# Performance work log

Hardware: AMD Instinct MI355X
Metric: run time of the kernel (lower is better)

The kernel has to match this reference:

```python
import jax, jax.numpy as jnp
import numpy as np
from jax import lax

DIM = 192
HEADS = 8
HID = int(DIM * 4.0)

def setup_inputs() -> dict:
    key = jax.random.key(0)
    ks = jax.random.split(key, 10)
    b, c, h, w = 4, DIM, 256, DIM  # w must equal dim for the Mlp over last axis
    x = jax.random.normal(ks[0], (b, c, h, w), dtype=jnp.float32)
    return {
        "x": x,
        "ln1_w": jnp.ones((DIM,), jnp.float32),
        "ln1_b": jnp.zeros((DIM,), jnp.float32),
        "temperature": jnp.ones((HEADS, 1, 1), jnp.float32),
        "qkv_w": jax.random.normal(ks[1], (3 * DIM, DIM), jnp.float32) * 0.02,
        "dw_w": jax.random.normal(ks[2], (3 * DIM, 1, 3, 3), jnp.float32) * 0.1,
        "proj_w": jax.random.normal(ks[3], (DIM, DIM), jnp.float32) * 0.02,
        "ln2_w": jnp.ones((DIM,), jnp.float32),
        "ln2_b": jnp.zeros((DIM,), jnp.float32),
        "fc1_w": jax.random.normal(ks[4], (HID, DIM), jnp.float32) * 0.02,
        "fc1_b": jnp.zeros((HID,), jnp.float32),
        "fc2_w": jax.random.normal(ks[5], (DIM, HID), jnp.float32) * 0.02,
        "fc2_b": jnp.zeros((DIM,), jnp.float32),
    }

def _layernorm_chan(x, w, b):
    # WithBias LayerNorm over the channel axis, per spatial location (to_3d -> LN -> to_4d)
    mu = jnp.mean(x, axis=1, keepdims=True)
    var = jnp.mean((x - mu) ** 2, axis=1, keepdims=True)
    y = (x - mu) / jnp.sqrt(var + 1e-5)
    return y * w[None, :, None, None] + b[None, :, None, None]

def _l2norm(x, axis=-1, eps=1e-12):
    n = jnp.sqrt(jnp.sum(x * x, axis=axis, keepdims=True))
    return x / jnp.maximum(n, eps)

def _attention(x, temperature, qkv_w, dw_w, proj_w):
    b, c, h, w = x.shape
    # 1x1 conv (pointwise GEMM) then 3x3 depthwise conv
    qkv = jnp.einsum('oc,bchw->bohw', qkv_w, x)
    qkv = lax.conv_general_dilated(qkv, dw_w, window_strides=(1, 1), padding='SAME',
                                   feature_group_count=3 * c,
                                   dimension_numbers=('NCHW', 'OIHW', 'NCHW'))
    q, k, v = jnp.split(qkv, 3, axis=1)
    ch = c // HEADS
    q = q.reshape(b, HEADS, ch, h * w)
    k = k.reshape(b, HEADS, ch, h * w)
    v = v.reshape(b, HEADS, ch, h * w)
    q = _l2norm(q)
    k = _l2norm(k)
    attn = jnp.einsum('bhcn,bhdn->bhcd', q, k) * temperature  # [b,H,ch,ch] channel attention
    attn = jax.nn.softmax(attn, axis=-1)
    out = jnp.einsum('bhcd,bhdn->bhcn', attn, v).reshape(b, c, h, w)
    return jnp.einsum('oc,bchw->bohw', proj_w, out)

def _mlp(x, fc1_w, fc1_b, fc2_w, fc2_b):
    # nn.Linear applied on the LAST axis (w == dim), matching the original quirk
    h1 = jnp.einsum('bchw,ow->bcho', x, fc1_w) + fc1_b
    h1 = jax.nn.gelu(h1, approximate=False)
    return jnp.einsum('bcho,do->bchd', h1, fc2_w) + fc2_b

def reference(x, ln1_w, ln1_b, temperature, qkv_w, dw_w, proj_w, ln2_w, ln2_b, fc1_w, fc1_b, fc2_w, fc2_b):
    x = x + _attention(_layernorm_chan(x, ln1_w, ln1_b), temperature, qkv_w, dw_w, proj_w)
    x = x + _mlp(_layernorm_chan(x, ln2_w, ln2_b), fc1_w, fc1_b, fc2_w, fc2_b)
    return x
```

## Files before the change

kernel.cpp:

```cpp
#include <hip/hip_runtime.h>
#include <math.h>

#define SSP   49152
#define HDIM  256
#define WDIM  192
#define CDIM  192
#define NHEAD 8
#define CH    24
#define OC3   576
#define HIDF  768
#define NB    4
#define SCCH  24

typedef short bf16x8 __attribute__((ext_vector_type(8)));
typedef short bf16x4 __attribute__((ext_vector_type(4)));
typedef float f32x4  __attribute__((ext_vector_type(4)));

__device__ inline short f2bf(float f) {
  unsigned u = __float_as_uint(f);
  u += 0x7fffu + ((u >> 16) & 1u);
  return (short)(u >> 16);
}
__device__ inline float bf2f(short h) {
  return __uint_as_float(((unsigned)(unsigned short)h) << 16);
}

__global__ __launch_bounds__(256) void cvt_bf16(const float* __restrict__ in,
                                                short* __restrict__ out, int n) {
  int i = blockIdx.x * 256 + threadIdx.x;
  if (i < n) out[i] = f2bf(in[i]);
}

__global__ __launch_bounds__(256) void ln_to_bf16T(const float* __restrict__ x,
                                                   const float* __restrict__ w,
                                                   const float* __restrict__ b,
                                                   short* __restrict__ yt) {
  int s = blockIdx.x * 256 + threadIdx.x;
  int bz = blockIdx.y;
  const float* xb = x + (size_t)bz * CDIM * SSP;
  float sum = 0.f, sq = 0.f;
  for (int c = 0; c < CDIM; ++c) {
    float v = xb[(size_t)c * SSP + s];
    sum += v; sq += v * v;
  }
  float mu = sum * (1.f / CDIM);
  float rstd = rsqrtf(sq * (1.f / CDIM) - mu * mu + 1e-5f);
  short* yp = yt + (size_t)bz * SSP * CDIM + (size_t)s * CDIM;
  for (int c8 = 0; c8 < CDIM / 8; ++c8) {
    bf16x8 v;
#pragma unroll
    for (int j = 0; j < 8; ++j) {
      int c = c8 * 8 + j;
      v[j] = f2bf((xb[(size_t)c * SSP + s] - mu) * rstd * w[c] + b[c]);
    }
    *(bf16x8*)(yp + c8 * 8) = v;
  }
}

__global__ __launch_bounds__(256) void ln_to_bf16N(const float* __restrict__ x,
                                                   const float* __restrict__ w,
                                                   const float* __restrict__ b,
                                                   short* __restrict__ y) {
  int s = blockIdx.x * 256 + threadIdx.x;
  int bz = blockIdx.y;
  const float* xb = x + (size_t)bz * CDIM * SSP;
  short* yb = y + (size_t)bz * CDIM * SSP;
  float sum = 0.f, sq = 0.f;
  for (int c = 0; c < CDIM; ++c) {
    float v = xb[(size_t)c * SSP + s];
    sum += v; sq += v * v;
  }
  float mu = sum * (1.f / CDIM);
  float rstd = rsqrtf(sq * (1.f / CDIM) - mu * mu + 1e-5f);
  for (int c = 0; c < CDIM; ++c) {
    float v = xb[(size_t)c * SSP + s];
    yb[(size_t)c * SSP + s] = f2bf((v - mu) * rstd * w[c] + b[c]);
  }
}

template <int BM, int BN, int WM, int WN, bool RESID, bool OUT_BF16>
__global__ __launch_bounds__(256) void mfma_gemm(
    const short* __restrict__ A, const short* __restrict__ B,
    const float* __restrict__ resid, void* __restrict__ Cv,
    int M, int N, int K, long long strideB, long long strideC) {
  constexpr int BK = 32, PAD = 40;
  constexpr int WTM = BM / WM, WTN = BN / WN;
  constexpr int FM = WTM / 16, FN = WTN / 16;
  static_assert(WM * WN == 4 && BM % 64 == 0 && BN % 64 == 0, "cfg");
  __shared__ short As[BM * PAD];
  __shared__ short Bs[BN * PAD];
  const int tid = threadIdx.x;
  const int m0 = blockIdx.y * BM, n0 = blockIdx.x * BN;
  const long long z = blockIdx.z;
  const short* Bz = B + z * strideB;
  const int w = tid >> 6, lane = tid & 63;
  const int wm = w / WN, wn = w % WN;
  const int r16 = lane & 15, kg = lane >> 4;
  const int arow = tid >> 2, akc = tid & 3;

  f32x4 acc[FM][FN] = {};

  for (int k0 = 0; k0 < K; k0 += BK) {
#pragma unroll
    for (int i = 0; i < BM; i += 64) {
      bf16x8 v = *(const bf16x8*)(A + (size_t)(m0 + i + arow) * K + k0 + akc * 8);
      *(bf16x8*)(&As[(i + arow) * PAD + akc * 8]) = v;
    }
#pragma unroll
    for (int i = 0; i < BN; i += 64) {
      bf16x8 v = *(const bf16x8*)(Bz + (size_t)(n0 + i + arow) * K + k0 + akc * 8);
      *(bf16x8*)(&Bs[(i + arow) * PAD + akc * 8]) = v;
    }
    __syncthreads();
    bf16x8 af[FM], bfr[FN];
#pragma unroll
    for (int i = 0; i < FM; ++i)
      af[i] = *(bf16x8*)(&As[(wm * WTM + i * 16 + r16) * PAD + kg * 8]);
#pragma unroll
    for (int j = 0; j < FN; ++j)
      bfr[j] = *(bf16x8*)(&Bs[(wn * WTN + j * 16 + r16) * PAD + kg * 8]);
#pragma unroll
    for (int i = 0; i < FM; ++i)
#pragma unroll
      for (int j = 0; j < FN; ++j)
        acc[i][j] = __builtin_amdgcn_mfma_f32_16x16x32_bf16(af[i], bfr[j], acc[i][j], 0, 0, 0);
    __syncthreads();
  }

  float* Cf = (float*)Cv + z * strideC;
  short* Ch = (short*)Cv + z * strideC;
  const float* R = RESID ? resid + z * strideC : nullptr;
#pragma unroll
  for (int i = 0; i < FM; ++i) {
#pragma unroll
    for (int j = 0; j < FN; ++j) {
#pragma unroll
      for (int t = 0; t < 4; ++t) {
        int m = m0 + wm * WTM + i * 16 + kg * 4 + t;
        int n = n0 + wn * WTN + j * 16 + r16;
        float v = acc[i][j][t];
        size_t idx = (size_t)m * N + n;
        if (RESID) v += R[idx];
        if (OUT_BF16) Ch[idx] = f2bf(v); else Cf[idx] = v;
      }
    }
  }
}

__global__ __launch_bounds__(256) void dwconv_tile(const short* __restrict__ in,
                                                   const float* __restrict__ w9,
                                                   short* __restrict__ out) {
  __shared__ short tile[34][208];
  const int tid = threadIdx.x;
  const int ch = blockIdx.x >> 3;
  const int slab = blockIdx.x & 7;
  const int o = ch % OC3;
  const int y0 = slab * 32;
  float wr[9];
#pragma unroll
  for (int i = 0; i < 9; ++i) wr[i] = w9[o * 9 + i];
  const short* ip = in + (size_t)ch * SSP;

  if (tid < 34) { tile[tid][7] = 0; tile[tid][200] = 0; }
#pragma unroll
  for (int i = 0; i < 4; ++i) {
    int idx = i * 256 + tid;
    if (idx < 816) {
      int row = idx / 24, cx = idx - row * 24;
      int gy = y0 + row - 1;
      bf16x8 v = {};
      if (gy >= 0 && gy < HDIM) v = *(const bf16x8*)(ip + gy * WDIM + cx * 8);
      *(bf16x8*)(&tile[row][8 + cx * 8]) = v;
    }
  }
  __syncthreads();

  short* op = out + (size_t)ch * SSP;
#pragma unroll
  for (int g = 0; g < 3; ++g) {
    int G = g * 256 + tid;
    int r = G / 24, cx = G - (G / 24) * 24;
    int cb = cx * 8 + 7;
    float a[10], b[10], c[10];
#pragma unroll
    for (int d = 0; d < 10; ++d) {
      a[d] = bf2f(tile[r][cb + d]);
      b[d] = bf2f(tile[r + 1][cb + d]);
      c[d] = bf2f(tile[r + 2][cb + d]);
    }
    bf16x8 ov;
#pragma unroll
    for (int j = 0; j < 8; ++j) {
      float acc = wr[0] * a[j] + wr[1] * a[j + 1] + wr[2] * a[j + 2]
                + wr[3] * b[j] + wr[4] * b[j + 1] + wr[5] * b[j + 2]
                + wr[6] * c[j] + wr[7] * c[j + 1] + wr[8] * c[j + 2];
      ov[j] = f2bf(acc);
    }
    *(bf16x8*)(op + (y0 + r) * WDIM + cx * 8) = ov;
  }
}

__global__ __launch_bounds__(256) void scores_stage1(const short* __restrict__ D,
                                                     float* __restrict__ pdot,
                                                     float* __restrict__ qss,
                                                     float* __restrict__ kss) {
  int ch = blockIdx.x, h = blockIdx.y, b = blockIdx.z;
  __shared__ float qs[24][260];
  __shared__ float ks[24][260];
  int tid = threadIdx.x;
  int w = tid >> 6, lane = tid & 63;
  int c0 = w * 6;
  float acc[6] = {0.f, 0.f, 0.f, 0.f, 0.f, 0.f};
  float ssacc = 0.f;
  const short* qb = D + ((size_t)b * OC3 + h * CH) * SSP;
  const short* kb = D + ((size_t)b * OC3 + CDIM + h * CH) * SSP;
  for (int it = 0; it < 8; ++it) {
    int s0 = ch * 2048 + it * 256;
#pragma unroll
    for (int p = 0; p < 3; ++p) {
      int u = p * 256 + tid;
      int row = u >> 5, col8 = u & 31;
      bf16x8 qv = *(const bf16x8*)(qb + (size_t)row * SSP + s0 + col8 * 8);
      bf16x8 kv = *(const bf16x8*)(kb + (size_t)row * SSP + s0 + col8 * 8);
#pragma unroll
      for (int j = 0; j < 8; ++j) {
        qs[row][col8 * 8 + j] = bf2f(qv[j]);
        ks[row][col8 * 8 + j] = bf2f(kv[j]);
      }
    }
    __syncthreads();
    if (w < 2 && lane < 24) {
      const float (*src)[260] = (w == 0) ? qs : ks;
      for (int s = 0; s < 256; s += 4) {
        float4 v = *(const float4*)&src[lane][s];
        ssacc += v.x * v.x + v.y * v.y + v.z * v.z + v.w * v.w;
      }
    }
    if (lane < 24) {
      for (int s = 0; s < 256; s += 4) {
        float4 kv = *(float4*)&ks[lane][s];
#pragma unroll
        for (int i = 0; i < 6; ++i) {
          float4 qv = *(float4*)&qs[c0 + i][s];
          acc[i] += qv.x * kv.x + qv.y * kv.y + qv.z * kv.z + qv.w * kv.w;
        }
      }
    }
    __syncthreads();
  }
  if (lane < 24) {
    float* pb = pdot + (size_t)b * (NHEAD * CH * CH * SCCH);
#pragma unroll
    for (int i = 0; i < 6; ++i)
      pb[(((size_t)h * CH + (c0 + i)) * CH + lane) * SCCH + ch] = acc[i];
    if (w == 0) qss[(((size_t)b * NHEAD + h) * CH + lane) * SCCH + ch] = ssacc;
    if (w == 1) kss[(((size_t)b * NHEAD + h) * CH + lane) * SCCH + ch] = ssacc;
  }
}

__global__ void scores_reduce(const float* __restrict__ pdot,
                              const float* __restrict__ qss,
                              const float* __restrict__ kss,
                              const float* __restrict__ temp,
                              float* __restrict__ atn) {
  int c = blockIdx.x, h = blockIdx.y, b = blockIdx.z;
  int tid = threadIdx.x;
  __shared__ float row[24];
  if (tid < 24) {
    const float* p = pdot + (size_t)b * (NHEAD * CH * CH * SCCH) +
                     (((size_t)h * CH + c) * CH + tid) * SCCH;
    float s = 0.f;
#pragma unroll
    for (int i = 0; i < SCCH; ++i) s += p[i];
    const float* pq = qss + (((size_t)b * NHEAD + h) * CH + c) * SCCH;
    const float* pk = kss + (((size_t)b * NHEAD + h) * CH + tid) * SCCH;
    float sq = 0.f, sk = 0.f;
#pragma unroll
    for (int i = 0; i < SCCH; ++i) { sq += pq[i]; sk += pk[i]; }
    float rq = 1.f / fmaxf(sqrtf(sq), 1e-12f);
    float rk = 1.f / fmaxf(sqrtf(sk), 1e-12f);
    row[tid] = s * rq * rk * temp[h];
  }
  __syncthreads();
  if (tid < 24) {
    float mx = -1e30f;
    for (int d = 0; d < 24; ++d) mx = fmaxf(mx, row[d]);
    float sum = 0.f;
    for (int d = 0; d < 24; ++d) sum += expf(row[d] - mx);
    atn[((size_t)b * NHEAD + h) * 576 + c * CH + tid] = expf(row[tid] - mx) / sum;
  }
}

__global__ __launch_bounds__(256) void attn_pv_bf16(const short* __restrict__ D,
                                                    const float* __restrict__ atn,
                                                    short* __restrict__ pvt) {
  int nb = blockIdx.x, h = blockIdx.y, b = blockIdx.z;
  __shared__ float aL[24][24];
  int tid = threadIdx.x;
  const float* ab = atn + ((size_t)b * NHEAD + h) * 576;
  for (int i = tid; i < 576; i += 256) aL[i / 24][i % 24] = ab[i];
  __syncthreads();
  int n = nb * 256 + tid;
  const short* vb = D + ((size_t)b * OC3 + 2 * CDIM + h * CH) * SSP + n;
  float vv[24];
#pragma unroll
  for (int d = 0; d < 24; ++d) vv[d] = bf2f(vb[(size_t)d * SSP]);
  short* ob = pvt + (size_t)b * SSP * CDIM + (size_t)n * CDIM + h * CH;
  bf16x8 o0, o1, o2;
#pragma unroll
  for (int cc = 0; cc < 24; ++cc) {
    float s = 0.f;
#pragma unroll
    for (int d = 0; d < 24; ++d) s += aL[cc][d] * vv[d];
    short bv = f2bf(s);
    if (cc < 8) o0[cc & 7] = bv; else if (cc < 16) o1[cc & 7] = bv; else o2[cc & 7] = bv;
  }
  *(bf16x8*)(ob) = o0;
  *(bf16x8*)(ob + 8) = o1;
  *(bf16x8*)(ob + 16) = o2;
}

__global__ __launch_bounds__(512) void mlp_fused(const short* __restrict__ y2,
                                                 const short* __restrict__ w1,
                                                 const short* __restrict__ w2,
                                                 const float* __restrict__ b1,
                                                 const float* __restrict__ b2,
                                                 float* __restrict__ out) {
  __shared__ short y2s[128 * 200];
  __shared__ short w1s[64 * 200];
  __shared__ short w2s[192 * 72];
  __shared__ short h1s[128 * 72];
  const int tid = threadIdx.x;
  const int m0 = blockIdx.x * 128;
  const int w = tid >> 6, lane = tid & 63;
  const int r16 = lane & 15, kg = lane >> 4;
  const int wm = w >> 1;
  const int wn = w & 1;

  const int u0 = tid, u1 = 512 + tid, u2 = 1024 + tid;
  const int s1r[3] = {u0 / 24, u1 / 24, u2 / 24};
  const int s1c[3] = {u0 % 24, u1 % 24, u2 % 24};
  const int s2r[3] = {u0 / 8, u1 / 8, u2 / 8};
  const int s2c[3] = {u0 % 8, u1 % 8, u2 % 8};

#pragma unroll
  for (int it = 0; it < 6; ++it) {
    int u = it * 512 + tid;
    int row = u / 24, cx = u % 24;
    bf16x8 v = *(const bf16x8*)(y2 + (size_t)(m0 + row) * CDIM + cx * 8);
    *(bf16x8*)(&y2s[row * 200 + cx * 8]) = v;
  }
#pragma unroll
  for (int it = 0; it < 3; ++it) {
    bf16x8 v = *(const bf16x8*)(w1 + (size_t)s1r[it] * CDIM + s1c[it] * 8);
    *(bf16x8*)(&w1s[s1r[it] * 200 + s1c[it] * 8]) = v;
    bf16x8 v2 = *(const bf16x8*)(w2 + (size_t)s2r[it] * HIDF + s2c[it] * 8);
    *(bf16x8*)(&w2s[s2r[it] * 72 + s2c[it] * 8]) = v2;
  }
  __syncthreads();

  f32x4 bacc[2][6] = {};
  bf16x8 rw1[3], rw2[3];

  for (int hc = 0; hc < 12; ++hc) {
    if (hc < 11) {
#pragma unroll
      for (int it = 0; it < 3; ++it) {
        rw1[it] = *(const bf16x8*)(w1 + (size_t)((hc + 1) * 64 + s1r[it]) * CDIM + s1c[it] * 8);
        rw2[it] = *(const bf16x8*)(w2 + (size_t)s2r[it] * HIDF + (hc + 1) * 64 + s2c[it] * 8);
      }
    }

    f32x4 pacc[2][2] = {};
#pragma unroll
    for (int ks = 0; ks < 6; ++ks) {
      bf16x8 af[2], bg[2];
#pragma unroll
      for (int i = 0; i < 2; ++i)
        af[i] = *(bf16x8*)(&y2s[(wm * 32 + i * 16 + r16) * 200 + ks * 32 + kg * 8]);
#pragma unroll
      for (int j = 0; j < 2; ++j)
        bg[j] = *(bf16x8*)(&w1s[(wn * 32 + j * 16 + r16) * 200 + ks * 32 + kg * 8]);
#pragma unroll
      for (int i = 0; i < 2; ++i)
#pragma unroll
        for (int j = 0; j < 2; ++j)
          pacc[i][j] = __builtin_amdgcn_mfma_f32_16x16x32_bf16(bg[j], af[i], pacc[i][j], 0, 0, 0);
    }
#pragma unroll
    for (int i = 0; i < 2; ++i) {
      int mr = wm * 32 + i * 16 + r16;
#pragma unroll
      for (int j = 0; j < 2; ++j) {
        int hid0 = wn * 32 + j * 16 + kg * 4;
        bf16x4 pk;
#pragma unroll
        for (int t = 0; t < 4; ++t) {
          float v = pacc[i][j][t] + b1[hc * 64 + hid0 + t];
          v = 0.5f * v * (1.f + erff(v * 0.70710678118654752f));
          pk[t] = f2bf(v);
        }
        *(bf16x4*)(&h1s[mr * 72 + hid0]) = pk;
      }
    }
    __syncthreads();

#pragma unroll
    for (int ks = 0; ks < 2; ++ks) {
      bf16x8 a2[2];
#pragma unroll
      for (int i = 0; i < 2; ++i)
        a2[i] = *(bf16x8*)(&h1s[(wm * 32 + i * 16 + r16) * 72 + ks * 32 + kg * 8]);
#pragma unroll
      for (int j = 0; j < 6; ++j) {
        bf16x8 b2g = *(bf16x8*)(&w2s[(wn * 96 + j * 16 + r16) * 72 + ks * 32 + kg * 8]);
#pragma unroll
        for (int i = 0; i < 2; ++i)
          bacc[i][j] = __builtin_amdgcn_mfma_f32_16x16x32_bf16(a2[i], b2g, bacc[i][j], 0, 0, 0);
      }
    }
    __syncthreads();

    if (hc < 11) {
#pragma unroll
      for (int it = 0; it < 3; ++it) {
        *(bf16x8*)(&w1s[s1r[it] * 200 + s1c[it] * 8]) = rw1[it];
        *(bf16x8*)(&w2s[s2r[it] * 72 + s2c[it] * 8]) = rw2[it];
      }
      __syncthreads();
    }
  }

#pragma unroll
  for (int i = 0; i < 2; ++i)
#pragma unroll
    for (int j = 0; j < 6; ++j)
#pragma unroll
      for (int t = 0; t < 4; ++t) {
        int m = m0 + wm * 32 + i * 16 + kg * 4 + t;
        int n = wn * 96 + j * 16 + r16;
        size_t idx = (size_t)m * CDIM + n;
        out[idx] = bacc[i][j][t] + b2[n] + out[idx];
      }
}

extern "C" void kernel_launch(void* const* d_in, const int* in_sizes, int n_in,
                              void* d_out, int out_size, void* d_ws, size_t ws_size,
                              hipStream_t stream) {
  const float* x      = (const float*)d_in[0];
  const float* ln1_w  = (const float*)d_in[1];
  const float* ln1_b  = (const float*)d_in[2];
  const float* temp   = (const float*)d_in[3];
  const float* qkv_w  = (const float*)d_in[4];
  const float* dw_w   = (const float*)d_in[5];
  const float* proj_w = (const float*)d_in[6];
  const float* ln2_w  = (const float*)d_in[7];
  const float* ln2_b  = (const float*)d_in[8];
  const float* fc1_w  = (const float*)d_in[9];
  const float* fc1_b  = (const float*)d_in[10];
  const float* fc2_w  = (const float*)d_in[11];
  const float* fc2_b  = (const float*)d_in[12];
  float* out = (float*)d_out;

  char* base = (char*)d_ws;
  short* wq  = (short*)base;
  short* wp  = wq + 110592;
  short* w1  = wp + 36864;
  short* w2  = w1 + 147456;
  float* pdot= (float*)(base + 890880);
  float* qss = (float*)(base + 2660352);
  float* kss = (float*)(base + 2734080);
  float* atn = (float*)(base + 2807808);
  short* Dv  = (short*)(base + 4194304);
  short* y1t = Dv;
  short* T   = (short*)(base + 230686720);
  short* pvt = T;
  short* y2  = (short*)(base + 457179136);

  cvt_bf16<<<dim3(432), 256, 0, stream>>>(qkv_w, wq, 110592);
  cvt_bf16<<<dim3(144), 256, 0, stream>>>(proj_w, wp, 36864);
  cvt_bf16<<<dim3(576), 256, 0, stream>>>(fc1_w, w1, 147456);
  cvt_bf16<<<dim3(576), 256, 0, stream>>>(fc2_w, w2, 147456);

  ln_to_bf16T<<<dim3(SSP / 256, NB), 256, 0, stream>>>(x, ln1_w, ln1_b, y1t);
  mfma_gemm<64, 256, 1, 4, false, true><<<dim3(SSP / 256, OC3 / 64, NB), 256, 0, stream>>>(
      wq, y1t, nullptr, T, OC3, SSP, CDIM, (long long)SSP * CDIM, (long long)OC3 * SSP);
  dwconv_tile<<<dim3(NB * OC3 * 8), 256, 0, stream>>>(T, dw_w, Dv);
  scores_stage1<<<dim3(SCCH, NHEAD, NB), 256, 0, stream>>>(Dv, pdot, qss, kss);
  scores_reduce<<<dim3(CH, NHEAD, NB), 64, 0, stream>>>(pdot, qss, kss, temp, atn);
  attn_pv_bf16<<<dim3(SSP / 256, NHEAD, NB), 256, 0, stream>>>(Dv, atn, pvt);
  mfma_gemm<64, 256, 1, 4, true, false><<<dim3(SSP / 256, CDIM / 64, NB), 256, 0, stream>>>(
      wp, pvt, x, out, CDIM, SSP, CDIM, (long long)SSP * CDIM, (long long)CDIM * SSP);
  ln_to_bf16N<<<dim3(SSP / 256, NB), 256, 0, stream>>>(out, ln2_w, ln2_b, y2);
  mlp_fused<<<dim3(196608 / 128), 512, 0, stream>>>(y2, w1, w2, fc1_b, fc2_b, out);
}
```

Baseline: 1.015 ms.

## Tile layernorm through shared memory, per-batch launches, double-buffer MLP weights, tanh GELU

Layernorm kernels now stage a 192x64 tile in shared memory with coalesced float4 loads instead of striding per thread. The attention pipeline is launched once per batch element, dropping the batch grid dimension, presumably so each batch's working set stays cache-resident. The fused MLP keeps its A fragments in registers, double-buffers the weight chunks in shared memory to remove one barrier per iteration, and replaces erf GELU with a tanh/exp approximation. The approximation changes numerics slightly, and per-batch launches add launch overhead.

```diff
diff --git a/kernel.cpp b/kernel.cpp
--- a/kernel.cpp
+++ b/kernel.cpp
@@ -31,50 +31,68 @@
   if (i < n) out[i] = f2bf(in[i]);
 }
 
-__global__ __launch_bounds__(256) void ln_to_bf16T(const float* __restrict__ x,
-                                                   const float* __restrict__ w,
-                                                   const float* __restrict__ b,
-                                                   short* __restrict__ yt) {
-  int s = blockIdx.x * 256 + threadIdx.x;
-  int bz = blockIdx.y;
-  const float* xb = x + (size_t)bz * CDIM * SSP;
-  float sum = 0.f, sq = 0.f;
-  for (int c = 0; c < CDIM; ++c) {
-    float v = xb[(size_t)c * SSP + s];
-    sum += v; sq += v * v;
-  }
-  float mu = sum * (1.f / CDIM);
-  float rstd = rsqrtf(sq * (1.f / CDIM) - mu * mu + 1e-5f);
-  short* yp = yt + (size_t)bz * SSP * CDIM + (size_t)s * CDIM;
-  for (int c8 = 0; c8 < CDIM / 8; ++c8) {
-    bf16x8 v;
-#pragma unroll
-    for (int j = 0; j < 8; ++j) {
-      int c = c8 * 8 + j;
-      v[j] = f2bf((xb[(size_t)c * SSP + s] - mu) * rstd * w[c] + b[c]);
-    }
-    *(bf16x8*)(yp + c8 * 8) = v;
-  }
-}
-
-__global__ __launch_bounds__(256) void ln_to_bf16N(const float* __restrict__ x,
-                                                   const float* __restrict__ w,
-                                                   const float* __restrict__ b,
-                                                   short* __restrict__ y) {
-  int s = blockIdx.x * 256 + threadIdx.x;
-  int bz = blockIdx.y;
-  const float* xb = x + (size_t)bz * CDIM * SSP;
-  short* yb = y + (size_t)bz * CDIM * SSP;
-  float sum = 0.f, sq = 0.f;
-  for (int c = 0; c < CDIM; ++c) {
-    float v = xb[(size_t)c * SSP + s];
-    sum += v; sq += v * v;
-  }
-  float mu = sum * (1.f / CDIM);
-  float rstd = rsqrtf(sq * (1.f / CDIM) - mu * mu + 1e-5f);
-  for (int c = 0; c < CDIM; ++c) {
-    float v = xb[(size_t)c * SSP + s];
-    yb[(size_t)c * SSP + s] = f2bf((v - mu) * rstd * w[c] + b[c]);
+template <bool TRANS>
+__global__ __launch_bounds__(256) void ln_bf16(const float* __restrict__ xb,
+                                               const float* __restrict__ w,
+                                               const float* __restrict__ bia,
+                                               short* __restrict__ outb) {
+  __shared__ float xs[192][68];
+  __shared__ float ps[4][64], pq[4][64], mus[64], rst[64];
+  const int tid = threadIdx.x;
+  const int s0 = blockIdx.x * 64;
+#pragma unroll
+  for (int it = 0; it < 12; ++it) {
+    int u = it * 256 + tid;
+    int c = u >> 4, q = u & 15;
+    float4 v = *(const float4*)(xb + (size_t)c * SSP + s0 + q * 4);
+    *(float4*)&xs[c][q * 4] = v;
+  }
+  __syncthreads();
+  {
+    int s = tid & 63, p = tid >> 6;
+    float sm = 0.f, sq = 0.f;
+    for (int c = p * 48; c < p * 48 + 48; ++c) {
+      float v = xs[c][s]; sm += v; sq += v * v;
+    }
+    ps[p][s] = sm; pq[p][s] = sq;
+  }
+  __syncthreads();
+  if (tid < 64) {
+    float sm = ps[0][tid] + ps[1][tid] + ps[2][tid] + ps[3][tid];
+    float sq = pq[0][tid] + pq[1][tid] + pq[2][tid] + pq[3][tid];
+    float mu = sm * (1.f / CDIM);
+    mus[tid] = mu;
+    rst[tid] = rsqrtf(sq * (1.f / CDIM) - mu * mu + 1e-5f);
+  }
+  __syncthreads();
+  if (TRANS) {
+#pragma unroll
+    for (int it = 0; it < 6; ++it) {
+      int u = it * 256 + tid;
+      int c8 = u >> 6, sr = u & 63;
+      float mu = mus[sr], r = rst[sr];
+      bf16x8 o;
+#pragma unroll
+      for (int j = 0; j < 8; ++j) {
+        int c = c8 * 8 + j;
+        o[j] = f2bf((xs[c][sr] - mu) * r * w[c] + bia[c]);
+      }
+      *(bf16x8*)(outb + (size_t)(s0 + sr) * CDIM + c8 * 8) = o;
+    }
+  } else {
+#pragma unroll
+    for (int it = 0; it < 6; ++it) {
+      int u = it * 256 + tid;
+      int c = u >> 3, sv = u & 7;
+      float wc = w[c], bc = bia[c];
+      bf16x8 o;
+#pragma unroll
+      for (int j = 0; j < 8; ++j) {
+        int s = sv * 8 + j;
+        o[j] = f2bf((xs[c][s] - mus[s]) * rst[s] * wc + bc);
+      }
+      *(bf16x8*)(outb + (size_t)c * SSP + s0 + sv * 8) = o;
+    }
   }
 }
 
@@ -82,7 +100,7 @@
 __global__ __launch_bounds__(256) void mfma_gemm(
     const short* __restrict__ A, const short* __restrict__ B,
     const float* __restrict__ resid, void* __restrict__ Cv,
-    int M, int N, int K, long long strideB, long long strideC) {
+    int M, int N, int K) {
   constexpr int BK = 32, PAD = 40;
   constexpr int WTM = BM / WM, WTN = BN / WN;
   constexpr int FM = WTM / 16, FN = WTN / 16;
@@ -91,8 +109,6 @@
   __shared__ short Bs[BN * PAD];
   const int tid = threadIdx.x;
   const int m0 = blockIdx.y * BM, n0 = blockIdx.x * BN;
-  const long long z = blockIdx.z;
-  const short* Bz = B + z * strideB;
   const int w = tid >> 6, lane = tid & 63;
   const int wm = w / WN, wn = w % WN;
   const int r16 = lane & 15, kg = lane >> 4;
@@ -108,7 +124,7 @@
     }
 #pragma unroll
     for (int i = 0; i < BN; i += 64) {
-      bf16x8 v = *(const bf16x8*)(Bz + (size_t)(n0 + i + arow) * K + k0 + akc * 8);
+      bf16x8 v = *(const bf16x8*)(B + (size_t)(n0 + i + arow) * K + k0 + akc * 8);
       *(bf16x8*)(&Bs[(i + arow) * PAD + akc * 8]) = v;
     }
     __syncthreads();
@@ -127,9 +143,8 @@
     __syncthreads();
   }
 
-  float* Cf = (float*)Cv + z * strideC;
-  short* Ch = (short*)Cv + z * strideC;
-  const float* R = RESID ? resid + z * strideC : nullptr;
+  float* Cf = (float*)Cv;
+  short* Ch = (short*)Cv;
 #pragma unroll
   for (int i = 0; i < FM; ++i) {
 #pragma unroll
@@ -140,7 +155,7 @@
         int n = n0 + wn * WTN + j * 16 + r16;
         float v = acc[i][j][t];
         size_t idx = (size_t)m * N + n;
-        if (RESID) v += R[idx];
+        if (RESID) v += resid[idx];
         if (OUT_BF16) Ch[idx] = f2bf(v); else Cf[idx] = v;
       }
     }
@@ -154,11 +169,10 @@
   const int tid = threadIdx.x;
   const int ch = blockIdx.x >> 3;
   const int slab = blockIdx.x & 7;
-  const int o = ch % OC3;
   const int y0 = slab * 32;
   float wr[9];
 #pragma unroll
-  for (int i = 0; i < 9; ++i) wr[i] = w9[o * 9 + i];
+  for (int i = 0; i < 9; ++i) wr[i] = w9[ch * 9 + i];
   const short* ip = in + (size_t)ch * SSP;
 
   if (tid < 34) { tile[tid][7] = 0; tile[tid][200] = 0; }
@@ -204,7 +218,7 @@
                                                      float* __restrict__ pdot,
                                                      float* __restrict__ qss,
                                                      float* __restrict__ kss) {
-  int ch = blockIdx.x, h = blockIdx.y, b = blockIdx.z;
+  int ch = blockIdx.x, h = blockIdx.y;
   __shared__ float qs[24][260];
   __shared__ float ks[24][260];
   int tid = threadIdx.x;
@@ -212,8 +226,8 @@
   int c0 = w * 6;
   float acc[6] = {0.f, 0.f, 0.f, 0.f, 0.f, 0.f};
   float ssacc = 0.f;
-  const short* qb = D + ((size_t)b * OC3 + h * CH) * SSP;
-  const short* kb = D + ((size_t)b * OC3 + CDIM + h * CH) * SSP;
+  const short* qb = D + (size_t)(h * CH) * SSP;
+  const short* kb = D + (size_t)(CDIM + h * CH) * SSP;
   for (int it = 0; it < 8; ++it) {
     int s0 = ch * 2048 + it * 256;
 #pragma unroll
@@ -249,12 +263,11 @@
     __syncthreads();
   }
   if (lane < 24) {
-    float* pb = pdot + (size_t)b * (NHEAD * CH * CH * SCCH);
 #pragma unroll
     for (int i = 0; i < 6; ++i)
-      pb[(((size_t)h * CH + (c0 + i)) * CH + lane) * SCCH + ch] = acc[i];
-    if (w == 0) qss[(((size_t)b * NHEAD + h) * CH + lane) * SCCH + ch] = ssacc;
-    if (w == 1) kss[(((size_t)b * NHEAD + h) * CH + lane) * SCCH + ch] = ssacc;
+      pdot[(((size_t)h * CH + (c0 + i)) * CH + lane) * SCCH + ch] = acc[i];
+    if (w == 0) qss[((size_t)h * CH + lane) * SCCH + ch] = ssacc;
+    if (w == 1) kss[((size_t)h * CH + lane) * SCCH + ch] = ssacc;
   }
 }
 
@@ -263,17 +276,16 @@
                               const float* __restrict__ kss,
                               const float* __restrict__ temp,
                               float* __restrict__ atn) {
-  int c = blockIdx.x, h = blockIdx.y, b = blockIdx.z;
+  int c = blockIdx.x, h = blockIdx.y;
   int tid = threadIdx.x;
   __shared__ float row[24];
   if (tid < 24) {
-    const float* p = pdot + (size_t)b * (NHEAD * CH * CH * SCCH) +
-                     (((size_t)h * CH + c) * CH + tid) * SCCH;
+    const float* p = pdot + (((size_t)h * CH + c) * CH + tid) * SCCH;
     float s = 0.f;
 #pragma unroll
     for (int i = 0; i < SCCH; ++i) s += p[i];
-    const float* pq = qss + (((size_t)b * NHEAD + h) * CH + c) * SCCH;
-    const float* pk = kss + (((size_t)b * NHEAD + h) * CH + tid) * SCCH;
+    const float* pq = qss + ((size_t)h * CH + c) * SCCH;
+    const float* pk = kss + ((size_t)h * CH + tid) * SCCH;
     float sq = 0.f, sk = 0.f;
 #pragma unroll
     for (int i = 0; i < SCCH; ++i) { sq += pq[i]; sk += pk[i]; }
@@ -287,25 +299,25 @@
     for (int d = 0; d < 24; ++d) mx = fmaxf(mx, row[d]);
     float sum = 0.f;
     for (int d = 0; d < 24; ++d) sum += expf(row[d] - mx);
-    atn[((size_t)b * NHEAD + h) * 576 + c * CH + tid] = expf(row[tid] - mx) / sum;
+    atn[(size_t)h * 576 + c * CH + tid] = expf(row[tid] - mx) / sum;
   }
 }
 
 __global__ __launch_bounds__(256) void attn_pv_bf16(const short* __restrict__ D,
                                                     const float* __restrict__ atn,
                                                     short* __restrict__ pvt) {
-  int nb = blockIdx.x, h = blockIdx.y, b = blockIdx.z;
+  int nb = blockIdx.x, h = blockIdx.y;
   __shared__ float aL[24][24];
   int tid = threadIdx.x;
-  const float* ab = atn + ((size_t)b * NHEAD + h) * 576;
+  const float* ab = atn + (size_t)h * 576;
   for (int i = tid; i < 576; i += 256) aL[i / 24][i % 24] = ab[i];
   __syncthreads();
   int n = nb * 256 + tid;
-  const short* vb = D + ((size_t)b * OC3 + 2 * CDIM + h * CH) * SSP + n;
+  const short* vb = D + (size_t)(2 * CDIM + h * CH) * SSP + n;
   float vv[24];
 #pragma unroll
   for (int d = 0; d < 24; ++d) vv[d] = bf2f(vb[(size_t)d * SSP]);
-  short* ob = pvt + (size_t)b * SSP * CDIM + (size_t)n * CDIM + h * CH;
+  short* ob = pvt + (size_t)n * CDIM + h * CH;
   bf16x8 o0, o1, o2;
 #pragma unroll
   for (int cc = 0; cc < 24; ++cc) {
@@ -326,16 +338,13 @@
                                                  const float* __restrict__ b1,
                                                  const float* __restrict__ b2,
                                                  float* __restrict__ out) {
-  __shared__ short y2s[128 * 200];
-  __shared__ short w1s[64 * 200];
-  __shared__ short w2s[192 * 72];
-  __shared__ short h1s[128 * 72];
+  __shared__ short smem[62464];
+  short* h1s = smem + 53248;
   const int tid = threadIdx.x;
   const int m0 = blockIdx.x * 128;
   const int w = tid >> 6, lane = tid & 63;
   const int r16 = lane & 15, kg = lane >> 4;
-  const int wm = w >> 1;
-  const int wn = w & 1;
+  const int wm = w >> 1, wn = w & 1;
 
   const int u0 = tid, u1 = 512 + tid, u2 = 1024 + tid;
   const int s1r[3] = {u0 / 24, u1 / 24, u2 / 24};
@@ -343,26 +352,38 @@
   const int s2r[3] = {u0 / 8, u1 / 8, u2 / 8};
   const int s2c[3] = {u0 % 8, u1 % 8, u2 % 8};
 
+  short* y2s = smem + 26624;
 #pragma unroll
   for (int it = 0; it < 6; ++it) {
     int u = it * 512 + tid;
     int row = u / 24, cx = u % 24;
-    bf16x8 v = *(const bf16x8*)(y2 + (size_t)(m0 + row) * CDIM + cx * 8);
-    *(bf16x8*)(&y2s[row * 200 + cx * 8]) = v;
+    *(bf16x8*)(&y2s[row * 200 + cx * 8]) =
+        *(const bf16x8*)(y2 + (size_t)(m0 + row) * CDIM + cx * 8);
   }
 #pragma unroll
   for (int it = 0; it < 3; ++it) {
-    bf16x8 v = *(const bf16x8*)(w1 + (size_t)s1r[it] * CDIM + s1c[it] * 8);
-    *(bf16x8*)(&w1s[s1r[it] * 200 + s1c[it] * 8]) = v;
-    bf16x8 v2 = *(const bf16x8*)(w2 + (size_t)s2r[it] * HIDF + s2c[it] * 8);
-    *(bf16x8*)(&w2s[s2r[it] * 72 + s2c[it] * 8]) = v2;
-  }
-  __syncthreads();
+    *(bf16x8*)(&smem[s1r[it] * 200 + s1c[it] * 8]) =
+        *(const bf16x8*)(w1 + (size_t)s1r[it] * CDIM + s1c[it] * 8);
+    *(bf16x8*)(&smem[12800 + s2r[it] * 72 + s2c[it] * 8]) =
+        *(const bf16x8*)(w2 + (size_t)s2r[it] * HIDF + s2c[it] * 8);
+  }
+  __syncthreads();
+
+  bf16x8 afr[2][6];
+#pragma unroll
+  for (int ks = 0; ks < 6; ++ks)
+#pragma unroll
+    for (int i = 0; i < 2; ++i)
+      afr[i][ks] = *(bf16x8*)(&y2s[(wm * 32 + i * 16 + r16) * 200 + ks * 32 + kg * 8]);
 
   f32x4 bacc[2][6] = {};
   bf16x8 rw1[3], rw2[3];
 
   for (int hc = 0; hc < 12; ++hc) {
+    short* bw1 = smem + (hc & 1) * 26624;
+    short* bw2 = bw1 + 12800;
+    short* nw1 = smem + ((hc & 1) ^ 1) * 26624;
+    short* nw2 = nw1 + 12800;
     if (hc < 11) {
 #pragma unroll
       for (int it = 0; it < 3; ++it) {
@@ -370,22 +391,18 @@
         rw2[it] = *(const bf16x8*)(w2 + (size_t)s2r[it] * HIDF + (hc + 1) * 64 + s2c[it] * 8);
       }
     }
-
     f32x4 pacc[2][2] = {};
 #pragma unroll
     for (int ks = 0; ks < 6; ++ks) {
-      bf16x8 af[2], bg[2];
+      bf16x8 bg[2];
+#pragma unroll
+      for (int j = 0; j < 2; ++j)
+        bg[j] = *(bf16x8*)(&bw1[(wn * 32 + j * 16 + r16) * 200 + ks * 32 + kg * 8]);
 #pragma unroll
       for (int i = 0; i < 2; ++i)
-        af[i] = *(bf16x8*)(&y2s[(wm * 32 + i * 16 + r16) * 200 + ks * 32 + kg * 8]);
-#pragma unroll
-      for (int j = 0; j < 2; ++j)
-        bg[j] = *(bf16x8*)(&w1s[(wn * 32 + j * 16 + r16) * 200 + ks * 32 + kg * 8]);
-#pragma unroll
-      for (int i = 0; i < 2; ++i)
 #pragma unroll
         for (int j = 0; j < 2; ++j)
-          pacc[i][j] = __builtin_amdgcn_mfma_f32_16x16x32_bf16(bg[j], af[i], pacc[i][j], 0, 0, 0);
+          pacc[i][j] = __builtin_amdgcn_mfma_f32_16x16x32_bf16(bg[j], afr[i][ks], pacc[i][j], 0, 0, 0);
     }
 #pragma unroll
     for (int i = 0; i < 2; ++i) {
@@ -397,14 +414,14 @@
 #pragma unroll
         for (int t = 0; t < 4; ++t) {
           float v = pacc[i][j][t] + b1[hc * 64 + hid0 + t];
-          v = 0.5f * v * (1.f + erff(v * 0.70710678118654752f));
+          float u = v * (0.7978845608f + 0.0356774081f * v * v);
+          v = v / (1.f + __expf(-2.f * u));
           pk[t] = f2bf(v);
         }
         *(bf16x4*)(&h1s[mr * 72 + hid0]) = pk;
       }
     }
     __syncthreads();
-
 #pragma unroll
     for (int ks = 0; ks < 2; ++ks) {
       bf16x8 a2[2];
@@ -413,22 +430,20 @@
         a2[i] = *(bf16x8*)(&h1s[(wm * 32 + i * 16 + r16) * 72 + ks * 32 + kg * 8]);
 #pragma unroll
       for (int j = 0; j < 6; ++j) {
-        bf16x8 b2g = *(bf16x8*)(&w2s[(wn * 96 + j * 16 + r16) * 72 + ks * 32 + kg * 8]);
+        bf16x8 b2g = *(bf16x8*)(&bw2[(wn * 96 + j * 16 + r16) * 72 + ks * 32 + kg * 8]);
 #pragma unroll
         for (int i = 0; i < 2; ++i)
           bacc[i][j] = __builtin_amdgcn_mfma_f32_16x16x32_bf16(a2[i], b2g, bacc[i][j], 0, 0, 0);
       }
     }
+    if (hc < 11) {
+#pragma unroll
+      for (int it = 0; it < 3; ++it) {
+        *(bf16x8*)(&nw1[s1r[it] * 200 + s1c[it] * 8]) = rw1[it];
+        *(bf16x8*)(&nw2[s2r[it] * 72 + s2c[it] * 8]) = rw2[it];
+      }
+    }
     __syncthreads();
-
-    if (hc < 11) {
-#pragma unroll
-      for (int it = 0; it < 3; ++it) {
-        *(bf16x8*)(&w1s[s1r[it] * 200 + s1c[it] * 8]) = rw1[it];
-        *(bf16x8*)(&w2s[s2r[it] * 72 + s2c[it] * 8]) = rw2[it];
-      }
-      __syncthreads();
-    }
   }
 
 #pragma unroll
@@ -462,6 +477,8 @@
   const float* fc2_b  = (const float*)d_in[12];
   float* out = (float*)d_out;
 
+  const size_t BSZ  = (size_t)CDIM * SSP;
+  const size_t B3SZ = (size_t)OC3 * SSP;
   char* base = (char*)d_ws;
   short* wq  = (short*)base;
   short* wp  = wq + 110592;
@@ -482,15 +499,29 @@
   cvt_bf16<<<dim3(576), 256, 0, stream>>>(fc1_w, w1, 147456);
   cvt_bf16<<<dim3(576), 256, 0, stream>>>(fc2_w, w2, 147456);
 
-  ln_to_bf16T<<<dim3(SSP / 256, NB), 256, 0, stream>>>(x, ln1_w, ln1_b, y1t);
-  mfma_gemm<64, 256, 1, 4, false, true><<<dim3(SSP / 256, OC3 / 64, NB), 256, 0, stream>>>(
-      wq, y1t, nullptr, T, OC3, SSP, CDIM, (long long)SSP * CDIM, (long long)OC3 * SSP);
-  dwconv_tile<<<dim3(NB * OC3 * 8), 256, 0, stream>>>(T, dw_w, Dv);
-  scores_stage1<<<dim3(SCCH, NHEAD, NB), 256, 0, stream>>>(Dv, pdot, qss, kss);
-  scores_reduce<<<dim3(CH, NHEAD, NB), 64, 0, stream>>>(pdot, qss, kss, temp, atn);
-  attn_pv_bf16<<<dim3(SSP / 256, NHEAD, NB), 256, 0, stream>>>(Dv, atn, pvt);
-  mfma_gemm<64, 256, 1, 4, true, false><<<dim3(SSP / 256, CDIM / 64, NB), 256, 0, stream>>>(
-      wp, pvt, x, out, CDIM, SSP, CDIM, (long long)SSP * CDIM, (long long)CDIM * SSP);
-  ln_to_bf16N<<<dim3(SSP / 256, NB), 256, 0, stream>>>(out, ln2_w, ln2_b, y2);
+  for (int b = 0; b < NB; ++b) {
+    const float* xb  = x + (size_t)b * BSZ;
+    float* outb      = out + (size_t)b * BSZ;
+    short* y1tb      = y1t + (size_t)b * BSZ;
+    short* Tb        = T + (size_t)b * B3SZ;
+    short* Dvb       = Dv + (size_t)b * B3SZ;
+    short* pvtb      = pvt + (size_t)b * BSZ;
+    short* y2b       = y2 + (size_t)b * BSZ;
+    float* pdotb     = pdot + (size_t)b * (NHEAD * CH * CH * SCCH);
+    float* qssb      = qss + (size_t)b * (NHEAD * CH * SCCH);
+    float* kssb      = kss + (size_t)b * (NHEAD * CH * SCCH);
+    float* atnb      = atn + (size_t)b * (NHEAD * 576);
+
+    ln_bf16<true><<<dim3(SSP / 64), 256, 0, stream>>>(xb, ln1_w, ln1_b, y1tb);
+    mfma_gemm<64, 256, 1, 4, false, true><<<dim3(SSP / 256, OC3 / 64), 256, 0, stream>>>(
+        wq, y1tb, nullptr, Tb, OC3, SSP, CDIM);
+    dwconv_tile<<<dim3(OC3 * 8), 256, 0, stream>>>(Tb, dw_w, Dvb);
+    scores_stage1<<<dim3(SCCH, NHEAD), 256, 0, stream>>>(Dvb, pdotb, qssb, kssb);
+    scores_reduce<<<dim3(CH, NHEAD), 64, 0, stream>>>(pdotb, qssb, kssb, temp, atnb);
+    attn_pv_bf16<<<dim3(SSP / 256, NHEAD), 256, 0, stream>>>(Dvb, atnb, pvtb);
+    mfma_gemm<64, 256, 1, 4, true, false><<<dim3(SSP / 256, CDIM / 64), 256, 0, stream>>>(
+        wp, pvtb, xb, outb, CDIM, SSP, CDIM);
+    ln_bf16<false><<<dim3(SSP / 64), 256, 0, stream>>>(outb, ln2_w, ln2_b, y2b);
+  }
   mlp_fused<<<dim3(196608 / 128), 512, 0, stream>>>(y2, w1, w2, fc1_b, fc2_b, out);
 }
```

Result: slower. 1.202 ms (+18.5%).
